# Kernel tuning notes

Hardware: AMD Instinct MI355X
Metric: run time of the kernel (lower is better)

Reference implementation:

```python
import jax, jax.numpy as jnp
import numpy as np

KEEP_RATIO = 0.8  # layer_threshold output at representative progress
NEG = -10000.0


def _extract(h, a, m):
    # h: [B,S,H] float, a: [B,S] float additive mask, m: [B,S] bool keep-mask
    # Torch version compacts to max_len = m.sum(-1).max(); here we pad the
    # compacted width to the static S (extra slots masked), same math.
    B, S, H = h.shape
    mi = m.astype(jnp.int32)
    c = jnp.cumsum(mi, axis=-1) * mi               # [B,S] dest slot (+1), 0 = dropped
    brow = jnp.arange(B)[:, None]
    amin = a.min()
    new_a = jnp.full((B, S + 1), amin, a.dtype).at[brow, c].set(a)[:, 1:]
    ar = jnp.broadcast_to(jnp.arange(S, dtype=jnp.int32), (B, S))
    index = jnp.full((B, S + 1), S, jnp.int32).at[brow, c].set(ar)[:, 1:]
    new_h = jnp.zeros((B, S + 1, H), h.dtype).at[brow, c].set(h)[:, 1:]
    return new_h, new_a, index


def _unextract(large, small, index):
    # scatter compacted `small` rows back into a copy of `large` at `index`;
    # index == S points at a sacrificial padded row that is dropped.
    B, S = large.shape[0], large.shape[1]
    brow = jnp.arange(B)[:, None]
    if large.ndim == 3:
        pad = jnp.zeros((B, 1, large.shape[2]), large.dtype)
    else:
        pad = jnp.zeros((B, 1), large.dtype)
    dest = jnp.concatenate([large, pad], axis=1)
    dest = dest.at[brow, index].set(small)
    return dest[:, :-1]


def _topk_mask(scores, attention_mask, keep_ratio):
    # keep top ceil-ish (tokens*ratio, >=1) scoring tokens per row
    B, S = scores.shape
    s = scores + attention_mask
    tokens = (attention_mask == 0).sum(1).astype(jnp.float32) * keep_ratio
    tokens = jnp.maximum(tokens.astype(jnp.int32), 1)            # [B]
    keep_first = jnp.arange(S, dtype=jnp.int32)[None, :] < tokens[:, None]
    order = jnp.argsort(-s, axis=1).astype(jnp.int32)            # descending sort indices
    idx = (order + 1) * keep_first.astype(jnp.int32)             # dropped -> slot 0
    brow = jnp.arange(B)[:, None]
    final = jnp.zeros((B, S + 1), jnp.float32).at[brow, idx].set(1.0)
    return final[:, 1:]


def setup_inputs() -> dict:
    key = jax.random.key(0)
    k1, k2, k3, k4 = jax.random.split(key, 4)
    B, S, H = 8, 4096, 1024
    hidden_states = jax.random.normal(k1, (B, S, H), dtype=jnp.float32)
    lengths = jax.random.randint(k2, (B,), S // 2, S + 1)
    valid = jnp.arange(S)[None, :] < lengths[:, None]
    attention_mask = jnp.where(valid, 0.0, NEG).astype(jnp.float32)
    keep = jax.random.uniform(k3, (B, S)) < 0.8
    previous_mask = (valid & keep).astype(jnp.float32).at[:, 0].set(1.0)
    W = (jax.random.normal(k4, (H, H), dtype=jnp.float32) / np.float32(np.sqrt(H)))
    b = jnp.zeros((H,), dtype=jnp.float32)
    return {"hidden_states": hidden_states, "attention_mask": attention_mask,
            "previous_mask": previous_mask, "W": W, "b": b}


def reference(hidden_states, attention_mask, previous_mask, W, b):
    m = previous_mask > 0.5
    sub_h, sub_a, sub_index = _extract(hidden_states, attention_mask, m)
    ret0 = sub_h  # child transformer layer abstracted to identity
    scores = jnp.max(jnp.einsum('bsh,hk->bsk', sub_h, W) + b, axis=-1) + sub_a * 100.0
    mask = _topk_mask(scores, sub_a, KEEP_RATIO)
    new_mask = _unextract(previous_mask, mask, sub_index)
    new_ret = _unextract(hidden_states, ret0, sub_index)
    return new_ret, new_mask
```

## Files before the change

kernel.cpp:

```cpp
#include <hip/hip_runtime.h>
#include <stdint.h>

static constexpr int BB = 8;
static constexpr int SS = 4096;
static constexpr int HH = 1024;

__device__ __forceinline__ unsigned f2mono(float f) {
    unsigned u = __float_as_uint(f);
    return (u & 0x80000000u) ? ~u : (u | 0x80000000u);
}
__device__ __forceinline__ float mono2f(unsigned u) {
    return __uint_as_float((u & 0x80000000u) ? (u ^ 0x80000000u) : ~u);
}

__global__ void k_init(const float* __restrict__ prev, unsigned* __restrict__ scores,
                       float* __restrict__ out_mask) {
    int i = blockIdx.x * blockDim.x + threadIdx.x;
    if (i < BB * SS) { scores[i] = 0u; out_mask[i] = prev[i]; }
}

__global__ void reduce_ab(const float* __restrict__ a, const float* __restrict__ bias,
                          float* __restrict__ amin_out, float* __restrict__ bmax_out) {
    __shared__ float red[256];
    int t = threadIdx.x;
    float mn = 1e30f;
    const float4* a4 = (const float4*)a;
    for (int i = t; i < BB * SS / 4; i += 256) {
        float4 v = a4[i];
        mn = fminf(mn, fminf(fminf(v.x, v.y), fminf(v.z, v.w)));
    }
    red[t] = mn; __syncthreads();
    for (int o = 128; o; o >>= 1) { if (t < o) red[t] = fminf(red[t], red[t + o]); __syncthreads(); }
    if (t == 0) *amin_out = red[0];
    __syncthreads();
    float mx = -1e30f;
    for (int i = t; i < HH; i += 256) mx = fmaxf(mx, bias[i]);
    red[t] = mx; __syncthreads();
    for (int o = 128; o; o >>= 1) { if (t < o) red[t] = fmaxf(red[t], red[t + o]); __syncthreads(); }
    if (t == 0) *bmax_out = red[0];
}

__global__ void compact(const float* __restrict__ prev, const float* __restrict__ a,
                        int* __restrict__ kept_src,
                        int* __restrict__ n_keep, int* __restrict__ zcnt) {
    int b = blockIdx.x;
    int lane = threadIdx.x;
    const float* pm = prev + (size_t)b * SS;
    const float* am = a + (size_t)b * SS;
    int* ks = kept_src + (size_t)b * SS;

    int base_s = lane * (SS / 64);
    int cnt = 0, zc = 0;
    for (int i = 0; i < SS / 64; ++i) {
        if (pm[base_s + i] > 0.5f) {
            cnt++;
            if (am[base_s + i] == 0.0f) zc++;
        }
    }
    int incl = cnt;
    for (int o = 1; o < 64; o <<= 1) {
        int v = __shfl_up(incl, o);
        if (lane >= o) incl += v;
    }
    int total = __shfl(incl, 63);
    int pos = incl - cnt;
    for (int i = 0; i < SS / 64; ++i) {
        if (pm[base_s + i] > 0.5f) ks[pos++] = base_s + i;
    }
    for (int o = 1; o < 64; o <<= 1) zc += __shfl_xor(zc, o);
    if (lane == 0) { n_keep[b] = total; zcnt[b] = zc; }
    for (int j = total + lane; j < SS; j += 64) ks[j] = 0;
}

#define BM 64
#define BN 256
#define BK 32
#define LDA 68
__global__ __launch_bounds__(256) void gemm_max(
    const float* __restrict__ hs, const float* __restrict__ W,
    const float* __restrict__ bias, const int* __restrict__ kept_src,
    const int* __restrict__ n_keep, unsigned* __restrict__ scores) {
    int mt = blockIdx.x, nt = blockIdx.y, b = blockIdx.z;
    int nk = n_keep[b];
    int m0 = mt * BM;
    if (m0 >= nk) return;

    __shared__ float A[BK][LDA];
    __shared__ int src[BM];
    int t = threadIdx.x;
    int lane = t & 63, w = t >> 6;
    if (t < BM) src[t] = kept_src[(size_t)b * SS + m0 + t];
    __syncthreads();

    int srow = t >> 2;
    int skq  = t & 3;
    const float* arow = hs + ((size_t)b * SS + (size_t)src[srow]) * HH + skq * 8;
    int n0 = nt * BN;
    const float* wcol = W + n0 + lane * 4;

    float acc[16][4];
#pragma unroll
    for (int r = 0; r < 16; ++r)
#pragma unroll
        for (int c = 0; c < 4; ++c) acc[r][c] = 0.f;

    for (int kc = 0; kc < HH / BK; ++kc) {
        float4 f0 = *(const float4*)(arow + kc * BK);
        float4 f1 = *(const float4*)(arow + kc * BK + 4);
        __syncthreads();
        int kb = skq * 8;
        A[kb + 0][srow] = f0.x; A[kb + 1][srow] = f0.y;
        A[kb + 2][srow] = f0.z; A[kb + 3][srow] = f0.w;
        A[kb + 4][srow] = f1.x; A[kb + 5][srow] = f1.y;
        A[kb + 6][srow] = f1.z; A[kb + 7][srow] = f1.w;
        __syncthreads();
        const float* wk = wcol + (size_t)kc * BK * HH;
#pragma unroll 4
        for (int k = 0; k < BK; ++k) {
            float4 w4 = *(const float4*)wk;
            wk += HH;
            const float4* ap = (const float4*)(&A[k][w * 16]);
            float4 a0 = ap[0], a1 = ap[1], a2 = ap[2], a3 = ap[3];
            float av[16] = {a0.x, a0.y, a0.z, a0.w, a1.x, a1.y, a1.z, a1.w,
                            a2.x, a2.y, a2.z, a2.w, a3.x, a3.y, a3.z, a3.w};
            float wv[4] = {w4.x, w4.y, w4.z, w4.w};
#pragma unroll
            for (int r = 0; r < 16; ++r)
#pragma unroll
                for (int c = 0; c < 4; ++c)
                    acc[r][c] = fmaf(av[r], wv[c], acc[r][c]);
        }
    }

    float4 bia = *(const float4*)(bias + n0 + lane * 4);
    float bv[4] = {bia.x, bia.y, bia.z, bia.w};
#pragma unroll
    for (int r = 0; r < 16; ++r) {
        float v = -1e30f;
#pragma unroll
        for (int c = 0; c < 4; ++c) v = fmaxf(v, acc[r][c] + bv[c]);
        for (int o = 32; o; o >>= 1) v = fmaxf(v, __shfl_xor(v, o));
        if (lane == 0)
            atomicMax(scores + (size_t)b * SS + m0 + w * 16 + r, f2mono(v));
    }
}

__global__ __launch_bounds__(1024) void topk_rank(
    const float* __restrict__ a, const int* __restrict__ kept_src,
    const unsigned* __restrict__ scores, const int* __restrict__ n_keep,
    const int* __restrict__ zcnt, const float* __restrict__ amin_p,
    const float* __restrict__ bmax_p, float* __restrict__ out_mask) {
    __shared__ unsigned long long keys[SS];
    int b = blockIdx.x, ch = blockIdx.y, t = threadIdx.x;
    int nk = n_keep[b];
    float amin = *amin_p, bmax = *bmax_p;
    int z = zcnt[b] + ((amin == 0.0f) ? (SS - nk) : 0);
    int tk = (int)((float)z * 0.8f);
    if (tk < 1) tk = 1;
    float padv = (bmax + amin * 100.0f) + amin;

    const int* ks = kept_src + (size_t)b * SS;
    const unsigned* sc = scores + (size_t)b * SS;
    const float* arow = a + (size_t)b * SS;

    for (int j = t; j < SS; j += 1024) {
        float sval;
        if (j < nk) {
            float core = mono2f(sc[j]);
            float av = arow[ks[j]];
            sval = (core + av * 100.0f) + av;
        } else {
            sval = padv;
        }
        keys[j] = ((unsigned long long)(~f2mono(sval)) << 32) | (unsigned)j;
    }
    __syncthreads();

    int j = ch * 1024 + t;
    unsigned long long mykey = keys[j];
    int rank = 0;
#pragma unroll 8
    for (int i = 0; i < SS; ++i) rank += (keys[i] < mykey) ? 1 : 0;

    if (j < nk) out_mask[(size_t)b * SS + ks[j]] = (rank < tk) ? 1.0f : 0.0f;
}

extern "C" void kernel_launch(void* const* d_in, const int* in_sizes, int n_in,
                              void* d_out, int out_size, void* d_ws, size_t ws_size,
                              hipStream_t stream) {
    const float* hs   = (const float*)d_in[0];
    const float* am   = (const float*)d_in[1];
    const float* pmsk = (const float*)d_in[2];
    const float* W    = (const float*)d_in[3];
    const float* bias = (const float*)d_in[4];

    float* out0 = (float*)d_out;
    float* out1 = out0 + (size_t)BB * SS * HH;

    char* ws = (char*)d_ws;
    int*      kept_src = (int*)ws;
    unsigned* scores   = (unsigned*)(ws + (size_t)BB * SS * 4);
    int*      nkeep    = (int*)(ws + (size_t)2 * BB * SS * 4);
    int*      zc       = nkeep + BB;
    float*    amin_p   = (float*)(zc + BB);
    float*    bmax_p   = amin_p + 1;

    hipMemcpyAsync(out0, hs, (size_t)BB * SS * HH * sizeof(float),
                   hipMemcpyDeviceToDevice, stream);

    hipLaunchKernelGGL(k_init, dim3(BB * SS / 256), dim3(256), 0, stream,
                       pmsk, scores, out1);
    hipLaunchKernelGGL(reduce_ab, dim3(1), dim3(256), 0, stream, am, bias, amin_p, bmax_p);
    hipLaunchKernelGGL(compact, dim3(BB), dim3(64), 0, stream,
                       pmsk, am, kept_src, nkeep, zc);
    hipLaunchKernelGGL(gemm_max, dim3(SS / BM, HH / BN, BB), dim3(256), 0, stream,
                       hs, W, bias, kept_src, nkeep, scores);
    hipLaunchKernelGGL(topk_rank, dim3(BB, SS / 1024), dim3(1024), 0, stream,
                       am, kept_src, scores, nkeep, zc, amin_p, bmax_p, out1);
}
```

Baseline: 999.4 us.

## Rewrite gemm_max as register-blocked direct-load GEMM and replace memcpy with blit kernel

The GEMM-max kernel drops its shared-memory A tile and the per-chunk barriers. Each wave now loads 8 gathered rows straight from global memory into registers, with the A and W loads double-buffered against the FMAs. The M tile shrinks from 64 to 32 rows, which doubles the grid, and launch bounds request one block per CU-slot. The device-to-device memcpy of the hidden states is replaced by a grid-stride float4 copy kernel. This trades shared-memory reuse of A for fewer syncs, but every wave now re-reads W from global or L2 with less reuse across rows.

```diff
diff --git a/kernel.cpp b/kernel.cpp
--- a/kernel.cpp
+++ b/kernel.cpp
@@ -11,6 +11,12 @@
 }
 __device__ __forceinline__ float mono2f(unsigned u) {
     return __uint_as_float((u & 0x80000000u) ? (u ^ 0x80000000u) : ~u);
+}
+
+__global__ void blit(const float4* __restrict__ s, float4* __restrict__ d, int n4) {
+    int i = blockIdx.x * blockDim.x + threadIdx.x;
+    int stride = gridDim.x * blockDim.x;
+    for (; i < n4; i += stride) d[i] = s[i];
 }
 
 __global__ void k_init(const float* __restrict__ prev, unsigned* __restrict__ scores,
@@ -72,77 +78,82 @@
     for (int j = total + lane; j < SS; j += 64) ks[j] = 0;
 }
 
-#define BM 64
-#define BN 256
-#define BK 32
-#define LDA 68
-__global__ __launch_bounds__(256) void gemm_max(
+#define MT 32
+#define NT 256
+__global__ __launch_bounds__(256, 1) void gemm_max(
     const float* __restrict__ hs, const float* __restrict__ W,
     const float* __restrict__ bias, const int* __restrict__ kept_src,
     const int* __restrict__ n_keep, unsigned* __restrict__ scores) {
     int mt = blockIdx.x, nt = blockIdx.y, b = blockIdx.z;
     int nk = n_keep[b];
-    int m0 = mt * BM;
+    int m0 = mt * MT;
     if (m0 >= nk) return;
 
-    __shared__ float A[BK][LDA];
-    __shared__ int src[BM];
-    int t = threadIdx.x;
-    int lane = t & 63, w = t >> 6;
-    if (t < BM) src[t] = kept_src[(size_t)b * SS + m0 + t];
-    __syncthreads();
-
-    int srow = t >> 2;
-    int skq  = t & 3;
-    const float* arow = hs + ((size_t)b * SS + (size_t)src[srow]) * HH + skq * 8;
-    int n0 = nt * BN;
+    int t = threadIdx.x, lane = t & 63, w = t >> 6;
+    int n0 = nt * NT;
+
+    const float* arow[8];
+#pragma unroll
+    for (int r = 0; r < 8; ++r) {
+        int src = kept_src[(size_t)b * SS + m0 + w * 8 + r];
+        arow[r] = hs + ((size_t)b * SS + (size_t)src) * HH;
+    }
     const float* wcol = W + n0 + lane * 4;
 
-    float acc[16][4];
-#pragma unroll
-    for (int r = 0; r < 16; ++r)
+    float acc[8][4];
+#pragma unroll
+    for (int r = 0; r < 8; ++r)
 #pragma unroll
         for (int c = 0; c < 4; ++c) acc[r][c] = 0.f;
 
-    for (int kc = 0; kc < HH / BK; ++kc) {
-        float4 f0 = *(const float4*)(arow + kc * BK);
-        float4 f1 = *(const float4*)(arow + kc * BK + 4);
-        __syncthreads();
-        int kb = skq * 8;
-        A[kb + 0][srow] = f0.x; A[kb + 1][srow] = f0.y;
-        A[kb + 2][srow] = f0.z; A[kb + 3][srow] = f0.w;
-        A[kb + 4][srow] = f1.x; A[kb + 5][srow] = f1.y;
-        A[kb + 6][srow] = f1.z; A[kb + 7][srow] = f1.w;
-        __syncthreads();
-        const float* wk = wcol + (size_t)kc * BK * HH;
-#pragma unroll 4
-        for (int k = 0; k < BK; ++k) {
-            float4 w4 = *(const float4*)wk;
-            wk += HH;
-            const float4* ap = (const float4*)(&A[k][w * 16]);
-            float4 a0 = ap[0], a1 = ap[1], a2 = ap[2], a3 = ap[3];
-            float av[16] = {a0.x, a0.y, a0.z, a0.w, a1.x, a1.y, a1.z, a1.w,
-                            a2.x, a2.y, a2.z, a2.w, a3.x, a3.y, a3.z, a3.w};
-            float wv[4] = {w4.x, w4.y, w4.z, w4.w};
-#pragma unroll
-            for (int r = 0; r < 16; ++r)
-#pragma unroll
-                for (int c = 0; c < 4; ++c)
-                    acc[r][c] = fmaf(av[r], wv[c], acc[r][c]);
-        }
+    float4 aC[8], aN[8], wC[4], wN[4];
+
+#define LOAD_STAGE(AV, WV, K4)                                             \
+    {                                                                      \
+        int _k4 = (K4);                                                    \
+        _Pragma("unroll")                                                  \
+        for (int r = 0; r < 8; ++r)                                        \
+            AV[r] = *(const float4*)(arow[r] + _k4 * 4);                   \
+        _Pragma("unroll")                                                  \
+        for (int kk = 0; kk < 4; ++kk)                                     \
+            WV[kk] = *(const float4*)(wcol + (size_t)(_k4 * 4 + kk) * HH); \
+    }
+
+#define COMPUTE_STAGE(AV, WV)                                              \
+    {                                                                      \
+        _Pragma("unroll")                                                  \
+        for (int kk = 0; kk < 4; ++kk) {                                   \
+            float wv0 = WV[kk].x, wv1 = WV[kk].y, wv2 = WV[kk].z, wv3 = WV[kk].w; \
+            _Pragma("unroll")                                              \
+            for (int r = 0; r < 8; ++r) {                                  \
+                float av = ((const float*)&AV[r])[kk];                     \
+                acc[r][0] = fmaf(av, wv0, acc[r][0]);                      \
+                acc[r][1] = fmaf(av, wv1, acc[r][1]);                      \
+                acc[r][2] = fmaf(av, wv2, acc[r][2]);                      \
+                acc[r][3] = fmaf(av, wv3, acc[r][3]);                      \
+            }                                                              \
+        }                                                                  \
+    }
+
+    LOAD_STAGE(aC, wC, 0)
+    for (int k4 = 0; k4 < HH / 4; k4 += 2) {
+        LOAD_STAGE(aN, wN, k4 + 1)
+        COMPUTE_STAGE(aC, wC)
+        LOAD_STAGE(aC, wC, (k4 + 2) & (HH / 4 - 1))
+        COMPUTE_STAGE(aN, wN)
     }
 
     float4 bia = *(const float4*)(bias + n0 + lane * 4);
-    float bv[4] = {bia.x, bia.y, bia.z, bia.w};
-#pragma unroll
-    for (int r = 0; r < 16; ++r) {
-        float v = -1e30f;
-#pragma unroll
-        for (int c = 0; c < 4; ++c) v = fmaxf(v, acc[r][c] + bv[c]);
+#pragma unroll
+    for (int r = 0; r < 8; ++r) {
+        float v = fmaxf(fmaxf(acc[r][0] + bia.x, acc[r][1] + bia.y),
+                        fmaxf(acc[r][2] + bia.z, acc[r][3] + bia.w));
         for (int o = 32; o; o >>= 1) v = fmaxf(v, __shfl_xor(v, o));
         if (lane == 0)
-            atomicMax(scores + (size_t)b * SS + m0 + w * 16 + r, f2mono(v));
-    }
+            atomicMax(scores + (size_t)b * SS + m0 + w * 8 + r, f2mono(v));
+    }
+#undef LOAD_STAGE
+#undef COMPUTE_STAGE
 }
 
 __global__ __launch_bounds__(1024) void topk_rank(
@@ -205,15 +216,15 @@
     float*    amin_p   = (float*)(zc + BB);
     float*    bmax_p   = amin_p + 1;
 
-    hipMemcpyAsync(out0, hs, (size_t)BB * SS * HH * sizeof(float),
-                   hipMemcpyDeviceToDevice, stream);
+    hipLaunchKernelGGL(blit, dim3(4096), dim3(256), 0, stream,
+                       (const float4*)hs, (float4*)out0, BB * SS * HH / 4);
 
     hipLaunchKernelGGL(k_init, dim3(BB * SS / 256), dim3(256), 0, stream,
                        pmsk, scores, out1);
     hipLaunchKernelGGL(reduce_ab, dim3(1), dim3(256), 0, stream, am, bias, amin_p, bmax_p);
     hipLaunchKernelGGL(compact, dim3(BB), dim3(64), 0, stream,
                        pmsk, am, kept_src, nkeep, zc);
-    hipLaunchKernelGGL(gemm_max, dim3(SS / BM, HH / BN, BB), dim3(256), 0, stream,
+    hipLaunchKernelGGL(gemm_max, dim3(SS / MT, HH / NT, BB), dim3(256), 0, stream,
                        hs, W, bias, kept_src, nkeep, scores);
     hipLaunchKernelGGL(topk_rank, dim3(BB, SS / 1024), dim3(1024), 0, stream,
                        am, kept_src, scores, nkeep, zc, amin_p, bmax_p, out1);
```

New measurement: 1.804 ms. 1.81x slower.
